# Optimization experiments

Measured on AMD Instinct MI355X. Metric: run time of the kernel, lower is better.

The kernel has to match this reference:

```python
import jax, jax.numpy as jnp
import numpy as np
import math

D_MODEL = 512
HEADS = 8
D_K = D_MODEL // HEADS
N_CODES = 2048
BETA = 0.2
# conv stack config: (in_ch, out_ch, kernel, stride)
CONV_CFG = [(105, 64, 10, 3), (64, 128, 3, 2), (128, 256, 3, 2),
            (256, 512, 3, 2), (512, 512, 2, 2), (512, 512, 2, 2)]


def setup_inputs() -> dict:
    key = jax.random.key(0)
    ks = jax.random.split(key, 32)
    inp = {"x": jax.random.normal(ks[0], (64, 105, 5500), dtype=jnp.float32)}
    # conv weights [out, in, k] (OIW layout) + biases, scaled ~ 1/sqrt(fan_in)
    for i, (cin, cout, k, s) in enumerate(CONV_CFG):
        std = 1.0 / math.sqrt(cin * k)
        inp[f"w{i+1}"] = jax.random.normal(ks[1 + 2 * i], (cout, cin, k), dtype=jnp.float32) * std
        inp[f"b{i+1}"] = jax.random.normal(ks[2 + 2 * i], (cout,), dtype=jnp.float32) * std
    # per-head Q/K/V projections stacked: [H, D, d_k]
    std = 1.0 / math.sqrt(D_MODEL)
    inp["wq"] = jax.random.normal(ks[13], (HEADS, D_MODEL, D_K), dtype=jnp.float32) * std
    inp["wk"] = jax.random.normal(ks[14], (HEADS, D_MODEL, D_K), dtype=jnp.float32) * std
    inp["wv"] = jax.random.normal(ks[15], (HEADS, D_MODEL, D_K), dtype=jnp.float32) * std
    inp["wo"] = jax.random.normal(ks[16], (D_MODEL, D_MODEL), dtype=jnp.float32) * std
    inp["bo"] = jax.random.normal(ks[17], (D_MODEL,), dtype=jnp.float32) * std
    # codebook (nn.Embedding default init ~ N(0,1))
    inp["codebook"] = jax.random.normal(ks[18], (N_CODES, D_MODEL), dtype=jnp.float32)
    return inp


def _conv_stack(x, ws, bs):
    # x: [B, C, T]; valid 1D convs with given strides
    for w, b, (_, _, _, s) in zip(ws, bs, CONV_CFG):
        x = jax.lax.conv_general_dilated(
            x, w, window_strides=(s,), padding='VALID',
            dimension_numbers=('NCH', 'OIH', 'NCH'))
        x = x + b[None, :, None]
    return x  # [B, 512, 57]


def _mha(x, wq, wk, wv, wo, bo):
    # x: [B, L, D]
    q = jnp.einsum('bld,hdk->bhlk', x, wq)
    k = jnp.einsum('bld,hdk->bhlk', x, wk)
    v = jnp.einsum('bld,hdk->bhlk', x, wv)
    scores = jnp.einsum('bhlk,bhmk->bhlm', q, k) / math.sqrt(D_K)
    attn = jax.nn.softmax(scores, axis=-1)
    out = jnp.einsum('bhlm,bhmk->bhlk', attn, v)
    B, H, L, dk = out.shape
    out = out.transpose(0, 2, 1, 3).reshape(B, L, H * dk)  # concat heads
    return out @ wo + bo


def reference(x, w1, b1, w2, b2, w3, b3, w4, b4, w5, b5, w6, b6,
              wq, wk, wv, wo, bo, codebook):
    ws = [w1, w2, w3, w4, w5, w6]
    bs = [b1, b2, b3, b4, b5, b6]
    conv_out = _conv_stack(x, ws, bs).transpose(0, 2, 1)  # [B, 57, 512]
    attn = _mha(conv_out, wq, wk, wv, wo, bo)             # [B, 57, 512]
    # squared Euclidean distances to codebook (same argmin as cdist)
    d2 = (jnp.sum(attn * attn, axis=-1, keepdims=True)    # [B, L, 1]
          - 2.0 * jnp.einsum('bld,nd->bln', attn, codebook)
          + jnp.sum(codebook * codebook, axis=-1)[None, None, :])  # [B, L, N]
    indices = jnp.argmin(d2, axis=-1)                     # [B, L]
    z_q = codebook[indices]                               # [B, L, D]
    codebook_loss = jnp.mean((z_q - jax.lax.stop_gradient(attn)) ** 2)
    commitment_loss = jnp.mean((attn - jax.lax.stop_gradient(z_q)) ** 2)
    vq_loss = codebook_loss + BETA * commitment_loss
    z_q_st = attn + jax.lax.stop_gradient(z_q - attn)
    return z_q_st, vq_loss, indices
```

## Files before the change

### kernel.cpp

```cpp
#include <hip/hip_runtime.h>
#include <hip/hip_bf16.h>
#include <math.h>

#define B_ 64
#define HB_ 32
#define L_ 57
#define D_ 512
#define H_ 8
#define DK_ 64
#define NC_ 2048

__global__ __launch_bounds__(256) void wtrans_k(const float* __restrict__ w,
                                                float* __restrict__ wT,
                                                int CINK, int COUT)
{
  int idx = blockIdx.x * 256 + threadIdx.x;
  if (idx >= CINK * COUT) return;
  int r = idx / COUT, c = idx - r * COUT;
  wT[idx] = w[(size_t)c * CINK + r];
}

__global__ __launch_bounds__(256) void wqkvprep_k(
    const float* __restrict__ wq, const float* __restrict__ wk,
    const float* __restrict__ wv, float* __restrict__ wqkvT)
{
  int idx = blockIdx.x * 256 + threadIdx.x;
  if (idx >= 786432) return;
  int set = idx >> 18;
  int h   = (idx >> 15) & 7;
  int d   = (idx >> 6) & 511;
  int kd  = idx & 63;
  const float* W = (set == 0 ? wq : (set == 1 ? wk : wv));
  float v = W[((size_t)h * 512 + d) * 64 + kd];
  wqkvT[(size_t)d * 1536 + set * 512 + h * 64 + kd] = v;
}

template<int CIN, int K, int S, int COUT, int CC>
__global__ __launch_bounds__(256, 4) void conv1d_k(
    const float* __restrict__ x, const float* __restrict__ wT,
    const float* __restrict__ bias, float* __restrict__ y,
    int Tin, int Tout)
{
  constexpr int TT = 64;
  constexpr int SPAN = S * TT + K - S;
  __shared__ float xs[CC * SPAN];
  const int b   = blockIdx.z;
  const int cbk = blockIdx.y;
  const int t0  = blockIdx.x * TT;
  const int tid = threadIdx.x;
  const int lane_t = tid & 63;
  const int g = tid >> 6;
  const int coutBase = __builtin_amdgcn_readfirstlane(cbk * 64 + g * 16);
  const int t = t0 + lane_t;
  float acc[16];
#pragma unroll
  for (int j = 0; j < 16; ++j) acc[j] = 0.f;
  const float* xb = x + (size_t)b * CIN * Tin;
  const int col0 = t0 * S;

  for (int c0 = 0; c0 < CIN; c0 += CC) {
    __syncthreads();
    for (int e = tid; e < CC * SPAN; e += 256) {
      int cc = e / SPAN, col = e - cc * SPAN;
      int ti = col0 + col;
      xs[e] = (ti < Tin) ? xb[(size_t)(c0 + cc) * Tin + ti] : 0.f;
    }
    __syncthreads();

    const float* wchunk = wT + ((size_t)c0 * K) * COUT + coutBase;
    for (int cc = 0; cc < CC; ++cc) {
#pragma unroll
      for (int kk = 0; kk < K; ++kk) {
        const float* wrow = wchunk + (size_t)(cc * K + kk) * COUT;
        float wv[16];
#pragma unroll
        for (int j = 0; j < 16; ++j) wv[j] = wrow[j];
        float xv = xs[cc * SPAN + lane_t * S + kk];
#pragma unroll
        for (int j = 0; j < 16; ++j) acc[j] += xv * wv[j];
      }
    }
  }
  if (t < Tout) {
#pragma unroll
    for (int j = 0; j < 16; ++j) {
      int co = coutBase + j;
      y[((size_t)b * COUT + co) * Tout + t] = acc[j] + bias[co];
    }
  }
}

template<int CIN, int K, int S, int COUT, int CC>
__global__ __launch_bounds__(256, 4) void conv1dw_k(
    const float* __restrict__ x, const float* __restrict__ wT,
    const float* __restrict__ bias, float* __restrict__ y,
    int Tin, int Tout)
{
  constexpr int TT = 128;
  constexpr int SPAN = S * TT + K - S;
  __shared__ float xs[CC * SPAN];
  const int b   = blockIdx.z;
  const int cbk = blockIdx.y;
  const int t0  = blockIdx.x * TT;
  const int tid = threadIdx.x;
  const int lane_t = tid & 63;
  const int g = tid >> 6;
  const int coutBase = __builtin_amdgcn_readfirstlane(cbk * 64 + g * 16);
  float acc0[16], acc1[16];
#pragma unroll
  for (int j = 0; j < 16; ++j) { acc0[j] = 0.f; acc1[j] = 0.f; }
  const float* xb = x + (size_t)b * CIN * Tin;
  const int col0 = t0 * S;

  for (int c0 = 0; c0 < CIN; c0 += CC) {
    __syncthreads();
    for (int e = tid; e < CC * SPAN; e += 256) {
      int cc = e / SPAN, col = e - cc * SPAN;
      int ti = col0 + col;
      xs[e] = (ti < Tin) ? xb[(size_t)(c0 + cc) * Tin + ti] : 0.f;
    }
    __syncthreads();

    const float* wchunk = wT + ((size_t)c0 * K) * COUT + coutBase;
    for (int cc = 0; cc < CC; ++cc) {
#pragma unroll
      for (int kk = 0; kk < K; ++kk) {
        const float* wrow = wchunk + (size_t)(cc * K + kk) * COUT;
        float wv[16];
#pragma unroll
        for (int j = 0; j < 16; ++j) wv[j] = wrow[j];
        float xv0 = xs[cc * SPAN + lane_t * S + kk];
        float xv1 = xs[cc * SPAN + (lane_t + 64) * S + kk];
#pragma unroll
        for (int j = 0; j < 16; ++j) {
          acc0[j] += xv0 * wv[j];
          acc1[j] += xv1 * wv[j];
        }
      }
    }
  }
  const int t_a = t0 + lane_t, t_b = t0 + 64 + lane_t;
#pragma unroll
  for (int j = 0; j < 16; ++j) {
    int co = coutBase + j;
    float bv = bias[co];
    float* yr = y + ((size_t)b * COUT + co) * Tout;
    if (t_a < Tout) yr[t_a] = acc0[j] + bv;
    if (t_b < Tout) yr[t_b] = acc1[j] + bv;
  }
}

template<int CINC, int K, int S, int COUT, int CC, int KS>
__global__ __launch_bounds__(256, 4) void convks_k(
    const float* __restrict__ x, const float* __restrict__ wT,
    float* __restrict__ p, int Tin, int Tout, int bStrideX, int ksStrideP)
{
  constexpr int TT = 64;
  constexpr int SPAN = S * TT + K - S;
  __shared__ float xs[CC * SPAN];
  const int b   = blockIdx.z;
  const int cbk = blockIdx.y & 7;
  const int ks  = blockIdx.y >> 3;
  const int t0  = blockIdx.x * TT;
  const int tid = threadIdx.x;
  const int lane_t = tid & 63;
  const int g = tid >> 6;
  const int coutBase = __builtin_amdgcn_readfirstlane(cbk * 64 + g * 16);
  const int t = t0 + lane_t;
  float acc[16];
#pragma unroll
  for (int j = 0; j < 16; ++j) acc[j] = 0.f;
  const float* xb = x + (size_t)b * bStrideX + (size_t)ks * CINC * Tin;
  const float* wbase = wT + ((size_t)ks * CINC * K) * COUT;
  const int col0 = t0 * S;

  for (int c0 = 0; c0 < CINC; c0 += CC) {
    __syncthreads();
    for (int e = tid; e < CC * SPAN; e += 256) {
      int cc = e / SPAN, col = e - cc * SPAN;
      int ti = col0 + col;
      xs[e] = (ti < Tin) ? xb[(size_t)(c0 + cc) * Tin + ti] : 0.f;
    }
    __syncthreads();

    const float* wchunk = wbase + ((size_t)c0 * K) * COUT + coutBase;
    for (int cc = 0; cc < CC; ++cc) {
#pragma unroll
      for (int kk = 0; kk < K; ++kk) {
        const float* wrow = wchunk + (size_t)(cc * K + kk) * COUT;
        float wv[16];
#pragma unroll
        for (int j = 0; j < 16; ++j) wv[j] = wrow[j];
        float xv = xs[cc * SPAN + lane_t * S + kk];
#pragma unroll
        for (int j = 0; j < 16; ++j) acc[j] += xv * wv[j];
      }
    }
  }
  if (t < Tout) {
#pragma unroll
    for (int j = 0; j < 16; ++j) {
      int co = coutBase + j;
      p[(size_t)ks * ksStrideP + ((size_t)b * COUT + co) * Tout + t] = acc[j];
    }
  }
}

template<int CINC, int K, int S, int COUT, int CC, int KS>
__global__ __launch_bounds__(256, 4) void convksw_k(
    const float* __restrict__ x, const float* __restrict__ wT,
    float* __restrict__ p, int Tin, int Tout, int bStrideX, int ksStrideP)
{
  constexpr int TT = 128;
  constexpr int SPAN = S * TT + K - S;
  __shared__ float xs[CC * SPAN];
  const int b   = blockIdx.z;
  const int cbk = blockIdx.y & 7;
  const int ks  = blockIdx.y >> 3;
  const int t0  = blockIdx.x * TT;
  const int tid = threadIdx.x;
  const int lane_t = tid & 63;
  const int g = tid >> 6;
  const int coutBase = __builtin_amdgcn_readfirstlane(cbk * 64 + g * 16);
  float acc0[16], acc1[16];
#pragma unroll
  for (int j = 0; j < 16; ++j) { acc0[j] = 0.f; acc1[j] = 0.f; }
  const float* xb = x + (size_t)b * bStrideX + (size_t)ks * CINC * Tin;
  const float* wbase = wT + ((size_t)ks * CINC * K) * COUT;
  const int col0 = t0 * S;

  for (int c0 = 0; c0 < CINC; c0 += CC) {
    __syncthreads();
    for (int e = tid; e < CC * SPAN; e += 256) {
      int cc = e / SPAN, col = e - cc * SPAN;
      int ti = col0 + col;
      xs[e] = (ti < Tin) ? xb[(size_t)(c0 + cc) * Tin + ti] : 0.f;
    }
    __syncthreads();

    const float* wchunk = wbase + ((size_t)c0 * K) * COUT + coutBase;
    for (int cc = 0; cc < CC; ++cc) {
#pragma unroll
      for (int kk = 0; kk < K; ++kk) {
        const float* wrow = wchunk + (size_t)(cc * K + kk) * COUT;
        float wv[16];
#pragma unroll
        for (int j = 0; j < 16; ++j) wv[j] = wrow[j];
        float xv0 = xs[cc * SPAN + lane_t * S + kk];
        float xv1 = xs[cc * SPAN + (lane_t + 64) * S + kk];
#pragma unroll
        for (int j = 0; j < 16; ++j) {
          acc0[j] += xv0 * wv[j];
          acc1[j] += xv1 * wv[j];
        }
      }
    }
  }
  const int t_a = t0 + lane_t, t_b = t0 + 64 + lane_t;
#pragma unroll
  for (int j = 0; j < 16; ++j) {
    int co = coutBase + j;
    float* pr = p + (size_t)ks * ksStrideP + ((size_t)b * COUT + co) * Tout;
    if (t_a < Tout) pr[t_a] = acc0[j];
    if (t_b < Tout) pr[t_b] = acc1[j];
  }
}

__global__ __launch_bounds__(256, 4) void convks6f_k(
    const float* __restrict__ pin, const float* __restrict__ wT,
    const float* __restrict__ b5, float* __restrict__ p,
    int p1Off, int ksStrideP)
{
  constexpr int CINC = 128, K = 2, S = 2, COUT = 512, CC = 32, TT = 64;
  constexpr int SPAN = S * TT + K - S;
  constexpr int TIN = 114;
  __shared__ float xs[CC * SPAN];
  const int b   = blockIdx.z;
  const int cbk = blockIdx.y & 7;
  const int ks  = blockIdx.y >> 3;
  const int t0  = blockIdx.x * TT;
  const int tid = threadIdx.x;
  const int lane_t = tid & 63;
  const int g = tid >> 6;
  const int coutBase = __builtin_amdgcn_readfirstlane(cbk * 64 + g * 16);
  const int t = t0 + lane_t;
  float acc[16];
#pragma unroll
  for (int j = 0; j < 16; ++j) acc[j] = 0.f;
  const float* wbase = wT + ((size_t)ks * CINC * K) * COUT;
  const int col0 = t0 * S;

  for (int c0 = 0; c0 < CINC; c0 += CC) {
    __syncthreads();
    for (int e = tid; e < CC * SPAN; e += 256) {
      int cc = e / SPAN, col = e - cc * SPAN;
      int ti = col0 + col;
      int gci = ks * CINC + c0 + cc;
      float v = 0.f;
      if (ti < TIN) {
        size_t off = (size_t)b * (512 * 114) + (size_t)gci * 114 + ti;
        v = pin[off] + pin[off + p1Off] + b5[gci];
      }
      xs[e] = v;
    }
    __syncthreads();

    const float* wchunk = wbase + ((size_t)c0 * K) * COUT + coutBase;
    for (int cc = 0; cc < CC; ++cc) {
#pragma unroll
      for (int kk = 0; kk < K; ++kk) {
        const float* wrow = wchunk + (size_t)(cc * K + kk) * COUT;
        float wv[16];
#pragma unroll
        for (int j = 0; j < 16; ++j) wv[j] = wrow[j];
        float xv = xs[cc * SPAN + lane_t * S + kk];
#pragma unroll
        for (int j = 0; j < 16; ++j) acc[j] += xv * wv[j];
      }
    }
  }
  if (t < 57) {
#pragma unroll
    for (int j = 0; j < 16; ++j) {
      int co = coutBase + j;
      p[(size_t)ks * ksStrideP + ((size_t)b * COUT + co) * 57 + t] = acc[j];
    }
  }
}

template<int COUT, int TOUT, int KS>
__global__ __launch_bounds__(256) void redbias_k(
    const float* __restrict__ p, const float* __restrict__ bias,
    float* __restrict__ y, int ksStride, int n)
{
  int idx = blockIdx.x * 256 + threadIdx.x;
  if (idx >= n) return;
  int c = (idx / TOUT) % COUT;
  float s = p[idx];
#pragma unroll
  for (int ks = 1; ks < KS; ++ks) s += p[idx + (size_t)ks * ksStride];
  y[idx] = s + bias[c];
}

__global__ __launch_bounds__(256) void itranspose_k(const float* __restrict__ y,
                                                    float* __restrict__ yT)
{
  const int b = blockIdx.y, dt = blockIdx.x;
  __shared__ float tile[32 * 58];
  const int tid = threadIdx.x;
  const int d0 = dt * 32;
  for (int e = tid; e < L_ * 32; e += 256) {
    int l = e >> 5, dd = e & 31;
    tile[dd * 58 + l] = y[((size_t)b * L_ + l) * D_ + d0 + dd];
  }
  __syncthreads();
  for (int e = tid; e < 32 * L_; e += 256) {
    int dd = e / L_, l = e - dd * L_;
    yT[((size_t)b * D_ + d0 + dd) * L_ + l] = tile[dd * 58 + l];
  }
}

__global__ __launch_bounds__(256, 2) void qkvgemm_k(
    const float* __restrict__ c6, const float* __restrict__ wqkvT,
    float* __restrict__ q, float* __restrict__ k, float* __restrict__ v)
{
  const int ot = blockIdx.x, b = blockIdx.y;
  const int tid = threadIdx.x;
  const int w = tid >> 6, lane = tid & 63;
  const int lrow = lane >> 3, ncol = lane & 7;
  __shared__ __align__(16) float As[32 * 68];
  __shared__ __align__(16) float Bs[32 * 256];
  float acc[8][8];
#pragma unroll
  for (int li = 0; li < 8; ++li)
#pragma unroll
    for (int nj = 0; nj < 8; ++nj) acc[li][nj] = 0.f;

  const float* c6b = c6 + (size_t)b * D_ * L_;
  const int o0 = ot * 256;

  for (int d0 = 0; d0 < D_; d0 += 32) {
    __syncthreads();
#pragma unroll
    for (int i = 0; i < 8; ++i) {
      int e = tid + i * 256;
      int dd = e >> 6, l = e & 63;
      As[dd * 68 + l] = (l < L_) ? c6b[(size_t)(d0 + dd) * L_ + l] : 0.f;
    }
#pragma unroll
    for (int i = 0; i < 8; ++i) {
      int e = tid + i * 256;
      int dd = e >> 6, o4 = (e & 63) * 4;
      *reinterpret_cast<float4*>(&Bs[dd * 256 + o4]) =
          *reinterpret_cast<const float4*>(&wqkvT[(size_t)(d0 + dd) * 1536 + o0 + o4]);
    }
    __syncthreads();
#pragma unroll 4
    for (int dd = 0; dd < 32; ++dd) {
      float a8[8], b8[8];
      *reinterpret_cast<float4*>(&a8[0]) = *reinterpret_cast<const float4*>(&As[dd * 68 + lrow * 8]);
      *reinterpret_cast<float4*>(&a8[4]) = *reinterpret_cast<const float4*>(&As[dd * 68 + lrow * 8 + 4]);
      *reinterpret_cast<float4*>(&b8[0]) = *reinterpret_cast<const float4*>(&Bs[dd * 256 + w * 64 + ncol * 8]);
      *reinterpret_cast<float4*>(&b8[4]) = *reinterpret_cast<const float4*>(&Bs[dd * 256 + w * 64 + ncol * 8 + 4]);
#pragma unroll
      for (int li = 0; li < 8; ++li)
#pragma unroll
        for (int nj = 0; nj < 8; ++nj)
          acc[li][nj] += a8[li] * b8[nj];
    }
  }

  const int o3 = o0 + w * 64 + ncol * 8;
  const int set = __builtin_amdgcn_readfirstlane(o3 >> 9);
  const int h = (o3 >> 6) & 7, kd = o3 & 63;
  float* OUT = (set == 0 ? q : (set == 1 ? k : v));
  float* base = OUT + (((size_t)b * H_ + h) * L_) * DK_ + kd;
#pragma unroll
  for (int li = 0; li < 8; ++li) {
    int l = lrow * 8 + li;
    if (l < L_) {
      float* p = base + (size_t)l * DK_;
      *reinterpret_cast<float4*>(p)     = *reinterpret_cast<float4*>(&acc[li][0]);
      *reinterpret_cast<float4*>(p + 4) = *reinterpret_cast<float4*>(&acc[li][4]);
    }
  }
}

__global__ __launch_bounds__(256) void attn_k(
    const float* __restrict__ q, const float* __restrict__ k, const float* __restrict__ v,
    float* __restrict__ cat)
{
  const int bh = blockIdx.x;
  const int b = bh >> 3, h = bh & 7;
  __shared__ float qs[L_ * DK_];
  __shared__ float ks[L_ * 65];
  __shared__ float vs[L_ * DK_];
  __shared__ float ps[L_ * DK_];
  const int tid = threadIdx.x;
  const float* qb = q + (size_t)bh * L_ * DK_;
  const float* kb = k + (size_t)bh * L_ * DK_;
  const float* vb = v + (size_t)bh * L_ * DK_;
  for (int e = tid; e < L_ * DK_; e += 256) {
    qs[e] = qb[e];
    vs[e] = vb[e];
    int m = e >> 6, d = e & 63;
    ks[m * 65 + d] = kb[e];
  }
  __syncthreads();
  for (int e = tid; e < L_ * L_; e += 256) {
    int l = e / L_, m = e - (e / L_) * L_;
    float s = 0.f;
#pragma unroll
    for (int d = 0; d < DK_; ++d) s += qs[l * DK_ + d] * ks[m * 65 + d];
    ps[l * DK_ + m] = s * 0.125f;
  }
  __syncthreads();
  if (tid < L_) {
    float mx = -1e30f;
    for (int m = 0; m < L_; ++m) mx = fmaxf(mx, ps[tid * DK_ + m]);
    float sum = 0.f;
    for (int m = 0; m < L_; ++m) { float e2 = __expf(ps[tid * DK_ + m] - mx); ps[tid * DK_ + m] = e2; sum += e2; }
    float inv = 1.f / sum;
    for (int m = 0; m < L_; ++m) ps[tid * DK_ + m] *= inv;
  }
  __syncthreads();
  for (int e = tid; e < L_ * DK_; e += 256) {
    int l = e >> 6, kd = e & 63;
    float s = 0.f;
    for (int m = 0; m < L_; ++m) s += ps[l * DK_ + m] * vs[m * DK_ + kd];
    cat[((size_t)b * L_ + l) * D_ + h * DK_ + kd] = s;
  }
}

__global__ __launch_bounds__(256) void outproj_k(
    const float* __restrict__ cat, const float* __restrict__ wo,
    const float* __restrict__ bo, float* __restrict__ y)
{
  const int b = blockIdx.y;
  const int lt = blockIdx.x >> 1;
  const int half = blockIdx.x & 1;
  const int l0 = lt * 16;
  const int o = half * 256 + threadIdx.x;
  __shared__ __align__(16) float cs[16 * D_];
  const int tid = threadIdx.x;
  for (int e = tid; e < 16 * D_; e += 256) {
    int l = l0 + (e >> 9);
    cs[e] = (l < L_) ? cat[((size_t)b * L_ + l) * D_ + (e & 511)] : 0.f;
  }
  __syncthreads();
  float acc[16];
#pragma unroll
  for (int j = 0; j < 16; ++j) acc[j] = 0.f;
  for (int d = 0; d < D_; d += 4) {
    float w0 = wo[(size_t)d * D_ + o];
    float w1 = wo[(size_t)(d + 1) * D_ + o];
    float w2 = wo[(size_t)(d + 2) * D_ + o];
    float w3 = wo[(size_t)(d + 3) * D_ + o];
#pragma unroll
    for (int j = 0; j < 16; ++j) {
      const float4 c4 = *reinterpret_cast<const float4*>(&cs[j * D_ + d]);
      acc[j] += c4.x * w0 + c4.y * w1 + c4.z * w2 + c4.w * w3;
    }
  }
  float bv = bo[o];
#pragma unroll
  for (int j = 0; j < 16; ++j) {
    int l = l0 + j;
    if (l < L_) y[((size_t)b * L_ + l) * D_ + o] = acc[j] + bv;
  }
}

__global__ __launch_bounds__(64) void cbprep_k(const float* __restrict__ cb,
                                               float* __restrict__ cbT,
                                               float* __restrict__ cnorm)
{
  const int n = blockIdx.x, t = threadIdx.x;
  float s = 0.f;
  for (int d = t; d < D_; d += 64) {
    float vv = cb[(size_t)n * D_ + d];
    cbT[(size_t)d * NC_ + n] = vv;
    s += vv * vv;
  }
#pragma unroll
  for (int off = 32; off >= 1; off >>= 1) s += __shfl_xor(s, off);
  if (t == 0) cnorm[n] = s;
}

__global__ __launch_bounds__(256, 2) void vqgemm_k(
    const float* __restrict__ yT, const float* __restrict__ cbT,
    const float* __restrict__ cnorm, float* __restrict__ pmin, int* __restrict__ pidx)
{
  const int b = blockIdx.y, nt = blockIdx.x;
  const int tid = threadIdx.x;
  const int w = tid >> 6, lane = tid & 63;
  const int lrow = lane >> 3, ncol = lane & 7;
  __shared__ __align__(16) float As[32 * 68];
  __shared__ __align__(16) float Bs[32 * 256];
  __shared__ float redv[4][64];
  __shared__ int   redi[4][64];
  float acc[8][8];
#pragma unroll
  for (int li = 0; li < 8; ++li)
#pragma unroll
    for (int nj = 0; nj < 8; ++nj) acc[li][nj] = 0.f;

  const float* yTb = yT + (size_t)b * D_ * L_;
  const int n0 = nt * 256;
  const int nbase = n0 + w * 64 + ncol * 8;

  for (int d0 = 0; d0 < D_; d0 += 32) {
    __syncthreads();
#pragma unroll
    for (int i = 0; i < 8; ++i) {
      int e = tid + i * 256;
      int dd = e >> 6, l = e & 63;
      As[dd * 68 + l] = (l < L_) ? yTb[(size_t)(d0 + dd) * L_ + l] : 0.f;
    }
#pragma unroll
    for (int i = 0; i < 8; ++i) {
      int e = tid + i * 256;
      int dd = e >> 6, n4 = (e & 63) * 4;
      *reinterpret_cast<float4*>(&Bs[dd * 256 + n4]) =
          *reinterpret_cast<const float4*>(&cbT[(size_t)(d0 + dd) * NC_ + n0 + n4]);
    }
    __syncthreads();
#pragma unroll 4
    for (int dd = 0; dd < 32; ++dd) {
      float a8[8], b8[8];
      *reinterpret_cast<float4*>(&a8[0]) = *reinterpret_cast<const float4*>(&As[dd * 68 + lrow * 8]);
      *reinterpret_cast<float4*>(&a8[4]) = *reinterpret_cast<const float4*>(&As[dd * 68 + lrow * 8 + 4]);
      *reinterpret_cast<float4*>(&b8[0]) = *reinterpret_cast<const float4*>(&Bs[dd * 256 + w * 64 + ncol * 8]);
      *reinterpret_cast<float4*>(&b8[4]) = *reinterpret_cast<const float4*>(&Bs[dd * 256 + w * 64 + ncol * 8 + 4]);
#pragma unroll
      for (int li = 0; li < 8; ++li)
#pragma unroll
        for (int nj = 0; nj < 8; ++nj)
          acc[li][nj] += a8[li] * b8[nj];
    }
  }

  float cn[8];
  *reinterpret_cast<float4*>(&cn[0]) = *reinterpret_cast<const float4*>(&cnorm[nbase]);
  *reinterpret_cast<float4*>(&cn[4]) = *reinterpret_cast<const float4*>(&cnorm[nbase + 4]);
#pragma unroll
  for (int li = 0; li < 8; ++li) {
    float vb = cn[0] - 2.f * acc[li][0];
    int ib = nbase;
#pragma unroll
    for (int nj = 1; nj < 8; ++nj) {
      float v = cn[nj] - 2.f * acc[li][nj];
      if (v < vb) { vb = v; ib = nbase + nj; }
    }
#pragma unroll
    for (int off = 1; off <= 4; off <<= 1) {
      float vo = __shfl_xor(vb, off);
      int io = __shfl_xor(ib, off);
      if (vo < vb || (vo == vb && io < ib)) { vb = vo; ib = io; }
    }
    if (ncol == 0) { redv[w][lrow * 8 + li] = vb; redi[w][lrow * 8 + li] = ib; }
  }
  __syncthreads();
  if (tid < L_) {
    float vb = redv[0][tid]; int ib = redi[0][tid];
#pragma unroll
    for (int w2 = 1; w2 < 4; ++w2) {
      float vo = redv[w2][tid]; int io = redi[w2][tid];
      if (vo < vb || (vo == vb && io < ib)) { vb = vo; ib = io; }
    }
    pmin[((size_t)b * L_ + tid) * 8 + nt] = vb;
    pidx[((size_t)b * L_ + tid) * 8 + nt] = ib;
  }
}

__global__ __launch_bounds__(64) void vqfin_k(
    const float* __restrict__ y, const float* __restrict__ cbook,
    const float* __restrict__ pmin, const int* __restrict__ pidx,
    float* __restrict__ zq, float* __restrict__ oidx, float* __restrict__ lpart)
{
  const int bl = blockIdx.x;
  const int tid = threadIdx.x;
  __shared__ int sidx;
  if (tid == 0) {
    float vb = pmin[(size_t)bl * 8];
    int ib = pidx[(size_t)bl * 8];
    for (int ntv = 1; ntv < 8; ++ntv) {
      float vo = pmin[(size_t)bl * 8 + ntv];
      int io = pidx[(size_t)bl * 8 + ntv];
      if (vo < vb || (vo == vb && io < ib)) { vb = vo; ib = io; }
    }
    sidx = ib;
  }
  __syncthreads();
  const int idx = sidx;
  const float* crow = cbook + (size_t)idx * D_;
  const float* yrow = y + (size_t)bl * D_;
  float s = 0.f;
  for (int d = tid; d < D_; d += 64) {
    float c = crow[d];
    float df = c - yrow[d];
    zq[(size_t)bl * D_ + d] = c;
    s += df * df;
  }
#pragma unroll
  for (int off = 32; off >= 1; off >>= 1) s += __shfl_xor(s, off);
  if (tid == 0) { lpart[bl] = s; oidx[bl] = (float)idx; }
}

__global__ __launch_bounds__(256) void loss_k(const float* __restrict__ lpart,
                                              float* __restrict__ outLoss)
{
  const int tid = threadIdx.x;
  float s = 0.f;
  for (int i = tid; i < B_ * L_; i += 256) s += lpart[i];
  __shared__ float red[256];
  red[tid] = s;
  __syncthreads();
  for (int off = 128; off >= 1; off >>= 1) {
    if (tid < off) red[tid] += red[tid + off];
    __syncthreads();
  }
  if (tid == 0) outLoss[0] = red[0] * ((1.f + 0.2f) / (float)((size_t)B_ * L_ * D_));
}

extern "C" void kernel_launch(void* const* d_in, const int* in_sizes, int n_in,
                              void* d_out, int out_size, void* d_ws, size_t ws_size,
                              hipStream_t stream)
{
  const float* x  = (const float*)d_in[0];
  const float* w1 = (const float*)d_in[1];  const float* b1 = (const float*)d_in[2];
  const float* w2 = (const float*)d_in[3];  const float* b2 = (const float*)d_in[4];
  const float* w3 = (const float*)d_in[5];  const float* b3 = (const float*)d_in[6];
  const float* w4 = (const float*)d_in[7];  const float* b4 = (const float*)d_in[8];
  const float* w5 = (const float*)d_in[9];  const float* b5 = (const float*)d_in[10];
  const float* w6 = (const float*)d_in[11]; const float* b6 = (const float*)d_in[12];
  const float* wq = (const float*)d_in[13];
  const float* wk = (const float*)d_in[14];
  const float* wv = (const float*)d_in[15];
  const float* wo = (const float*)d_in[16];
  const float* bo = (const float*)d_in[17];
  const float* cbook = (const float*)d_in[18];

  float* ws = (float*)d_ws;
  float* wT1 = ws;
  float* wT2 = ws + 67200;
  float* wT3 = ws + 91776;
  float* wT4 = ws + 190080;
  float* wT5 = ws + 583296;
  float* wT6 = ws + 1107584;

  const bool FULL = (ws_size >= (size_t)18507840 * 4);

  wtrans_k<<<(1050 * 64 + 255) / 256, 256, 0, stream>>>(w1, wT1, 1050, 64);
  wtrans_k<<<( 192 * 128 + 255) / 256, 256, 0, stream>>>(w2, wT2, 192, 128);
  wtrans_k<<<( 384 * 256 + 255) / 256, 256, 0, stream>>>(w3, wT3, 384, 256);
  wtrans_k<<<( 768 * 512 + 255) / 256, 256, 0, stream>>>(w4, wT4, 768, 512);
  wtrans_k<<<(1024 * 512 + 255) / 256, 256, 0, stream>>>(w5, wT5, 1024, 512);
  wtrans_k<<<(1024 * 512 + 255) / 256, 256, 0, stream>>>(w6, wT6, 1024, 512);

  float* c6;
  if (FULL) {
    float* P = ws + 1640000;
    float* Q = ws + 9140032;
    c6 = ws + 16640064;
    conv1dw_k<105,10,3, 64,21><<<dim3(15,1,B_),256,0,stream>>>(x, wT1,b1, P, 5500,1831);
    conv1dw_k< 64, 3,2,128,32><<<dim3( 8,2,B_),256,0,stream>>>(P, wT2,b2, Q, 1831, 915);
    conv1dw_k<128, 3,2,256,32><<<dim3( 4,4,B_),256,0,stream>>>(Q, wT3,b3, P,  915, 457);
    conv1dw_k<256, 3,2,512,32><<<dim3( 2,8,B_),256,0,stream>>>(P, wT4,b4, Q,  457, 228);
    convksw_k<256,2,2,512,32,2><<<dim3(1,16,B_),256,0,stream>>>(
        Q, wT5, P, 228, 114, 512 * 228, 3735552);
    convks6f_k<<<dim3(1,32,B_),256,0,stream>>>(P, wT6, b5, Q, 3735552, 1867776);
    redbias_k<512,57,4><<<(1867776 + 255) / 256, 256, 0, stream>>>(
        Q, b6, c6, 1867776, 1867776);
  } else {
    float* bufA = ws + 1632000;
    float* bufB = ws + 5382016;
    c6 = ws + 9132032;
    for (int h = 0; h < 2; ++h) {
      const float* xh = x + (size_t)h * HB_ * 105 * 5500;
      float* c6h = c6 + (size_t)h * HB_ * D_ * L_;
      conv1d_k<105,10,3, 64,21><<<dim3(29,1,HB_),256,0,stream>>>(xh,   wT1,b1, bufA, 5500,1831);
      conv1d_k< 64, 3,2,128,32><<<dim3(15,2,HB_),256,0,stream>>>(bufA, wT2,b2, bufB, 1831, 915);
      conv1d_k<128, 3,2,256,32><<<dim3( 8,4,HB_),256,0,stream>>>(bufB, wT3,b3, bufA,  915, 457);
      conv1d_k<256, 3,2,512,32><<<dim3( 4,8,HB_),256,0,stream>>>(bufA, wT4,b4, bufB,  457, 228);
      convks_k<256,2,2,512,32,2><<<dim3(2,16,HB_),256,0,stream>>>(
          bufB, wT5, bufA, 228, 114, 512 * 228, 1867776);
      convks6f_k<<<dim3(1,32,HB_),256,0,stream>>>(
          bufA, wT6, b5, bufB, 1867776, 933888);
      redbias_k<512,57,4><<<(933888 + 255) / 256, 256, 0, stream>>>(
          bufB, b6, c6h, 933888, 933888);
    }
  }

  float* qb     = ws;
  float* kb     = ws + 1867776;
  float* vb     = ws + 3735552;
  float* wqkvT  = ws + 5603328;
  float* cat    = ws + 7471104;
  float* yattn  = ws;
  float* yT     = ws + 1867776;
  float* cbT    = ws + 11206656;
  float* cnorm  = ws + 12255232;
  float* pminb  = ws + 12257280;
  int*   pidxb  = (int*)(ws + 12286464);
  float* lpart  = ws + 12315648;

  float* zq      = (float*)d_out;
  float* outLoss = zq + (size_t)B_ * L_ * D_;
  float* outIdx  = outLoss + 1;

  wqkvprep_k<<<(786432 + 255) / 256, 256, 0, stream>>>(wq, wk, wv, wqkvT);
  qkvgemm_k<<<dim3(6, B_), 256, 0, stream>>>(c6, wqkvT, qb, kb, vb);
  cbprep_k<<<NC_, 64, 0, stream>>>(cbook, cbT, cnorm);
  attn_k<<<B_ * H_, 256, 0, stream>>>(qb, kb, vb, cat);
  outproj_k<<<dim3(8, B_), 256, 0, stream>>>(cat, wo, bo, yattn);

  itranspose_k<<<dim3(16, B_), 256, 0, stream>>>(yattn, yT);
  vqgemm_k<<<dim3(8, B_), 256, 0, stream>>>(yT, cbT, cnorm, pminb, pidxb);
  vqfin_k<<<B_ * L_, 64, 0, stream>>>(yattn, cbook, pminb, pidxb, zq, outIdx, lpart);
  loss_k<<<1, 256, 0, stream>>>(lpart, outLoss);
}
```

Before: 1.194 ms.

## Split first conv layer over input channels with partial-sum reduction

Replaces the single conv1 kernel with a split-K version that divides the 105 input channels into two halves (padded to 112 with zero weights) and writes partial outputs, followed by a reduction kernel that sums the partials and adds the bias. This doubles the block count for the first layer, which previously launched only 15x64 blocks, to improve occupancy and parallelism. In exchange it writes and rereads an extra partial buffer and adds a launch. Workspace offsets shift to fit the padded weight matrix.

Result: no change. 1.194 ms (+0.0%).

```diff
diff --git a/kernel.cpp b/kernel.cpp
--- a/kernel.cpp
+++ b/kernel.cpp
@@ -18,6 +18,16 @@
   if (idx >= CINK * COUT) return;
   int r = idx / COUT, c = idx - r * COUT;
   wT[idx] = w[(size_t)c * CINK + r];
+}
+
+__global__ __launch_bounds__(256) void wtransp_k(const float* __restrict__ w,
+                                                 float* __restrict__ wT,
+                                                 int CINK, int CINK_PAD, int COUT)
+{
+  int idx = blockIdx.x * 256 + threadIdx.x;
+  if (idx >= CINK_PAD * COUT) return;
+  int r = idx / COUT, c = idx - r * COUT;
+  wT[idx] = (r < CINK) ? w[(size_t)c * CINK + r] : 0.f;
 }
 
 __global__ __launch_bounds__(256) void wqkvprep_k(
@@ -147,6 +157,67 @@
     float* yr = y + ((size_t)b * COUT + co) * Tout;
     if (t_a < Tout) yr[t_a] = acc0[j] + bv;
     if (t_b < Tout) yr[t_b] = acc1[j] + bv;
+  }
+}
+
+__global__ __launch_bounds__(256, 4) void conv1ksw_k(
+    const float* __restrict__ x, const float* __restrict__ wT,
+    float* __restrict__ p, int ksStrideP)
+{
+  constexpr int K = 10, S = 3, COUT = 64, CC = 14, TT = 128;
+  constexpr int SPAN = S * TT + K - S;
+  constexpr int TIN = 5500, TOUT = 1831, CINTOT = 105;
+  __shared__ float xs[CC * SPAN];
+  const int b  = blockIdx.z;
+  const int ks = blockIdx.y;
+  const int t0 = blockIdx.x * TT;
+  const int tid = threadIdx.x;
+  const int lane_t = tid & 63;
+  const int g = tid >> 6;
+  const int coutBase = __builtin_amdgcn_readfirstlane(g * 16);
+  float acc0[16], acc1[16];
+#pragma unroll
+  for (int j = 0; j < 16; ++j) { acc0[j] = 0.f; acc1[j] = 0.f; }
+  const float* xb = x + (size_t)b * CINTOT * TIN;
+  const int col0 = t0 * S;
+
+#pragma unroll
+  for (int c0i = 0; c0i < 4; ++c0i) {
+    const int cin0 = ks * 56 + c0i * CC;
+    __syncthreads();
+    for (int e = tid; e < CC * SPAN; e += 256) {
+      int cc = e / SPAN, col = e - cc * SPAN;
+      int gci = cin0 + cc;
+      int ti = col0 + col;
+      xs[e] = (ti < TIN && gci < CINTOT) ? xb[(size_t)gci * TIN + ti] : 0.f;
+    }
+    __syncthreads();
+
+    const float* wchunk = wT + ((size_t)cin0 * K) * COUT + coutBase;
+    for (int cc = 0; cc < CC; ++cc) {
+#pragma unroll
+      for (int kk = 0; kk < K; ++kk) {
+        const float* wrow = wchunk + (size_t)(cc * K + kk) * COUT;
+        float wv[16];
+#pragma unroll
+        for (int j = 0; j < 16; ++j) wv[j] = wrow[j];
+        float xv0 = xs[cc * SPAN + lane_t * S + kk];
+        float xv1 = xs[cc * SPAN + (lane_t + 64) * S + kk];
+#pragma unroll
+        for (int j = 0; j < 16; ++j) {
+          acc0[j] += xv0 * wv[j];
+          acc1[j] += xv1 * wv[j];
+        }
+      }
+    }
+  }
+  const int t_a = t0 + lane_t, t_b = t0 + 64 + lane_t;
+#pragma unroll
+  for (int j = 0; j < 16; ++j) {
+    int co = coutBase + j;
+    float* pr = p + (size_t)ks * ksStrideP + ((size_t)b * COUT + co) * TOUT;
+    if (t_a < TOUT) pr[t_a] = acc0[j];
+    if (t_b < TOUT) pr[t_b] = acc1[j];
   }
 }
 
@@ -682,15 +753,15 @@
 
   float* ws = (float*)d_ws;
   float* wT1 = ws;
-  float* wT2 = ws + 67200;
-  float* wT3 = ws + 91776;
-  float* wT4 = ws + 190080;
-  float* wT5 = ws + 583296;
-  float* wT6 = ws + 1107584;
+  float* wT2 = ws + 71680;
+  float* wT3 = ws + 96256;
+  float* wT4 = ws + 194560;
+  float* wT5 = ws + 587776;
+  float* wT6 = ws + 1112064;
 
   const bool FULL = (ws_size >= (size_t)18507840 * 4);
 
-  wtrans_k<<<(1050 * 64 + 255) / 256, 256, 0, stream>>>(w1, wT1, 1050, 64);
+  wtransp_k<<<(1120 * 64 + 255) / 256, 256, 0, stream>>>(w1, wT1, 1050, 1120, 64);
   wtrans_k<<<( 192 * 128 + 255) / 256, 256, 0, stream>>>(w2, wT2, 192, 128);
   wtrans_k<<<( 384 * 256 + 255) / 256, 256, 0, stream>>>(w3, wT3, 384, 256);
   wtrans_k<<<( 768 * 512 + 255) / 256, 256, 0, stream>>>(w4, wT4, 768, 512);
@@ -702,7 +773,9 @@
     float* P = ws + 1640000;
     float* Q = ws + 9140032;
     c6 = ws + 16640064;
-    conv1dw_k<105,10,3, 64,21><<<dim3(15,1,B_),256,0,stream>>>(x, wT1,b1, P, 5500,1831);
+    conv1ksw_k<<<dim3(15,2,B_),256,0,stream>>>(x, wT1, P, 7500032);
+    redbias_k<64,1831,2><<<(7499776 + 255) / 256, 256, 0, stream>>>(
+        P, b1, P, 7500032, 7499776);
     conv1dw_k< 64, 3,2,128,32><<<dim3( 8,2,B_),256,0,stream>>>(P, wT2,b2, Q, 1831, 915);
     conv1dw_k<128, 3,2,256,32><<<dim3( 4,4,B_),256,0,stream>>>(Q, wT3,b3, P,  915, 457);
     conv1dw_k<256, 3,2,512,32><<<dim3( 2,8,B_),256,0,stream>>>(P, wT4,b4, Q,  457, 228);
@@ -712,9 +785,9 @@
     redbias_k<512,57,4><<<(1867776 + 255) / 256, 256, 0, stream>>>(
         Q, b6, c6, 1867776, 1867776);
   } else {
-    float* bufA = ws + 1632000;
-    float* bufB = ws + 5382016;
-    c6 = ws + 9132032;
+    float* bufA = ws + 1640000;
+    float* bufB = ws + 5390016;
+    c6 = ws + 9140032;
     for (int h = 0; h < 2; ++h) {
       const float* xh = x + (size_t)h * HB_ * 105 * 5500;
       float* c6h = c6 + (size_t)h * HB_ * D_ * L_;
```
